# Performance work log

Hardware: AMD Instinct MI355X
Metric: run time of the kernel (lower is better)

The kernel has to match this reference:

```python
import jax, jax.numpy as jnp
import numpy as np

B, M, D, P, T = 512, 16, 128, 16, 4096
GAMMA = 1.0  # similarity_size


def setup_inputs() -> dict:
    key = jax.random.key(0)
    k1, k2, k3, k4, k5 = jax.random.split(key, 5)
    phi = jax.random.normal(k1, (B, P), dtype=jnp.float32)
    state = jax.random.normal(k2, (B, D), dtype=jnp.float32)
    trajectories = jax.random.normal(k3, (T, D), dtype=jnp.float32)
    # Stand-in per-model KAARMA state-transition parameters (linear recurrent + input map, tanh)
    A = jax.random.normal(k4, (M, D, D), dtype=jnp.float32) * (1.0 / np.sqrt(D))
    B_in = jax.random.normal(k5, (M, P, D), dtype=jnp.float32) * (1.0 / np.sqrt(P))
    return {"phi": phi, "state": state, "trajectories": trajectories, "A": A, "B_in": B_in}


def reference(phi, state, trajectories, A, B_in):
    # per-model state update: new_state[b,m,:] = tanh(state @ A_m + phi @ B_m)
    new_state = jnp.tanh(
        jnp.einsum("bd,mdh->bmh", state, A) + jnp.einsum("bp,mph->bmh", phi, B_in)
    )  # [B, M, D]
    # RBF similarity vs trajectory set via ||s||^2 + ||t||^2 - 2 s.t (single batched GEMM)
    s_sq = jnp.sum(new_state * new_state, axis=-1, keepdims=True)      # [B, M, 1]
    t_sq = jnp.sum(trajectories * trajectories, axis=-1)               # [T]
    cross = jnp.einsum("bmd,td->bmt", new_state, trajectories)         # [B, M, T]
    sq_dist = jnp.maximum(s_sq + t_sq[None, None, :] - 2.0 * cross, 0.0)
    sim = jnp.exp(-GAMMA * sq_dist)                                    # [B, M, T]
    output = sim.reshape(phi.shape[0], -1)                             # [B, M*T]
    return output, new_state
```

## Files before the change

kernel.cpp:

```cpp
#include <hip/hip_runtime.h>
#include <hip/hip_bf16.h>
#include <cstdint>
#include <cstddef>

#define NB 512
#define NM 16
#define ND 128
#define NP 16
#define NT 4096

typedef __bf16 bf16x8 __attribute__((ext_vector_type(8)));
typedef float f32x4 __attribute__((ext_vector_type(4)));

static_assert(sizeof(bf16x8) == 16, "bf16x8 must be 16B");

__device__ __forceinline__ void gload_lds16(const void* g, void* l) {
  __builtin_amdgcn_global_load_lds(
      (const __attribute__((address_space(1))) unsigned int*)g,
      (__attribute__((address_space(3))) unsigned int*)l, 16, 0, 0);
}

__global__ __launch_bounds__(256) void prep_kernel(
    const float* __restrict__ phi, const float* __restrict__ state,
    const float* __restrict__ traj, const float* __restrict__ A,
    const float* __restrict__ Bin, float* __restrict__ ns_out,
    __bf16* __restrict__ ns_bf, __bf16* __restrict__ tj_bf,
    float* __restrict__ s_sq, float* __restrict__ t_sq) {
  __shared__ alignas(16) float sSt[16 * 128];
  __shared__ alignas(16) float sPhi[16 * 16];
  __shared__ alignas(16) float sRes[16 * 128];
  const int tid = threadIdx.x;
  const int bx = blockIdx.x;

  if (bx < 512) {
    const int m = bx & 15;
    const int b0 = (bx >> 4) * 16;
    const float4* S4 = (const float4*)(state + (size_t)b0 * 128);
    float4* sSt4 = (float4*)sSt;
    sSt4[tid] = S4[tid];
    sSt4[tid + 256] = S4[tid + 256];
    sPhi[tid] = phi[b0 * 16 + tid];
    __syncthreads();

    const int h2 = tid & 63;
    const int rgrp = tid >> 6;
    const float* Ap = A + (size_t)m * 16384 + h2;
    const float* Bp = Bin + (size_t)m * 2048 + h2;

    float acc[2][4];
#pragma unroll
    for (int hi = 0; hi < 2; ++hi)
#pragma unroll
      for (int j = 0; j < 4; ++j) acc[hi][j] = 0.f;

#pragma unroll 4
    for (int c = 0; c < 32; ++c) {
      float a0[4], a1[4];
#pragma unroll
      for (int u = 0; u < 4; ++u) {
        a0[u] = Ap[(size_t)(c * 4 + u) * 128];
        a1[u] = Ap[(size_t)(c * 4 + u) * 128 + 64];
      }
#pragma unroll
      for (int j = 0; j < 4; ++j) {
        const f32x4 sv = *(const f32x4*)&sSt[(rgrp * 4 + j) * 128 + c * 4];
#pragma unroll
        for (int u = 0; u < 4; ++u) {
          acc[0][j] = fmaf(sv[u], a0[u], acc[0][j]);
          acc[1][j] = fmaf(sv[u], a1[u], acc[1][j]);
        }
      }
    }
#pragma unroll
    for (int pc = 0; pc < 4; ++pc) {
      float b0v[4], b1v[4];
#pragma unroll
      for (int u = 0; u < 4; ++u) {
        b0v[u] = Bp[(size_t)(pc * 4 + u) * 128];
        b1v[u] = Bp[(size_t)(pc * 4 + u) * 128 + 64];
      }
#pragma unroll
      for (int j = 0; j < 4; ++j) {
        const f32x4 pv = *(const f32x4*)&sPhi[(rgrp * 4 + j) * 16 + pc * 4];
#pragma unroll
        for (int u = 0; u < 4; ++u) {
          acc[0][j] = fmaf(pv[u], b0v[u], acc[0][j]);
          acc[1][j] = fmaf(pv[u], b1v[u], acc[1][j]);
        }
      }
    }

#pragma unroll
    for (int j = 0; j < 4; ++j) {
      const int row = rgrp * 4 + j;
      const int R = (b0 + row) * 16 + m;
      const float v0 = tanhf(acc[0][j]);
      const float v1 = tanhf(acc[1][j]);
      ns_out[(size_t)R * 128 + h2] = v0;
      ns_out[(size_t)R * 128 + h2 + 64] = v1;
      sRes[row * 128 + h2] = v0;
      sRes[row * 128 + h2 + 64] = v1;
      float s = v0 * v0 + v1 * v1;
#pragma unroll
      for (int o = 32; o > 0; o >>= 1) s += __shfl_xor(s, o);
      if (h2 == 0) s_sq[R] = s;
    }
    __syncthreads();

    {
      const int row = tid >> 4;
      const int kb = tid & 15;
      const f32x4 r0 = *(const f32x4*)&sRes[row * 128 + kb * 8];
      const f32x4 r1 = *(const f32x4*)&sRes[row * 128 + kb * 8 + 4];
      bf16x8 o;
#pragma unroll
      for (int i = 0; i < 4; ++i) {
        o[i] = (__bf16)r0[i];
        o[i + 4] = (__bf16)r1[i];
      }
      const int R = (b0 + row) * 16 + m;
      *(bf16x8*)(ns_bf + (size_t)R * 128 + ((kb ^ m) * 8)) = o;
    }
  } else {
    const int t0 = (bx - 512) * 128;
    const int t = t0 + (tid >> 1);
    const int half = tid & 1;
    float s = 0.f;
#pragma unroll
    for (int q = 0; q < 8; ++q) {
      const int kb = half * 8 + q;
      const f32x4 v0 = *(const f32x4*)&traj[(size_t)t * 128 + kb * 8];
      const f32x4 v1 = *(const f32x4*)&traj[(size_t)t * 128 + kb * 8 + 4];
      s += v0[0] * v0[0] + v0[1] * v0[1] + v0[2] * v0[2] + v0[3] * v0[3];
      s += v1[0] * v1[0] + v1[1] * v1[1] + v1[2] * v1[2] + v1[3] * v1[3];
      bf16x8 o;
#pragma unroll
      for (int i = 0; i < 4; ++i) {
        o[i] = (__bf16)v0[i];
        o[i + 4] = (__bf16)v1[i];
      }
      *(bf16x8*)(tj_bf + (size_t)t * 128 + ((kb ^ (t & 15)) * 8)) = o;
    }
    s += __shfl_xor(s, 1);
    if (half == 0) t_sq[t] = s;
  }
}

__global__ __launch_bounds__(256) void sim_kernel(
    const __bf16* __restrict__ ns_bf, const __bf16* __restrict__ tj_bf,
    const float* __restrict__ s_sq, const float* __restrict__ t_sq,
    float* __restrict__ out) {
  __shared__ alignas(16) __bf16 sA[128 * 128];
  __shared__ alignas(16) __bf16 sB[128 * 128];
  __shared__ float sSq[128];
  __shared__ float sTq[128];
  const int tid = threadIdx.x;
  const int lane = tid & 63;
  const int w = tid >> 6;
  const int R0 = blockIdx.x * 128;
  const int C0 = blockIdx.y * 128;

  const char* gA = (const char*)(ns_bf + (size_t)R0 * 128);
  const char* gB = (const char*)(tj_bf + (size_t)C0 * 128);
#pragma unroll
  for (int it = 0; it < 8; ++it) {
    const int off = it * 4096 + w * 1024;
    gload_lds16(gA + off + lane * 16, (char*)sA + off);
    gload_lds16(gB + off + lane * 16, (char*)sB + off);
  }
  if (tid < 128)
    sSq[tid] = s_sq[R0 + tid];
  else
    sTq[tid - 128] = t_sq[C0 + tid - 128];
  __syncthreads();

  const int rbase = (w >> 1) * 64;
  const int cbase = (w & 1) * 64;
  const int l15 = lane & 15;
  const int quad = lane >> 4;

  f32x4 acc[4][4];
#pragma unroll
  for (int i = 0; i < 4; ++i)
#pragma unroll
    for (int j = 0; j < 4; ++j) acc[i][j] = (f32x4){0.f, 0.f, 0.f, 0.f};

#pragma unroll
  for (int ks = 0; ks < 4; ++ks) {
    const int kb = quad + ks * 4;
    const int koff = (kb ^ l15) * 8;
    bf16x8 af[4], bfr[4];
#pragma unroll
    for (int i = 0; i < 4; ++i)
      af[i] = *(const bf16x8*)&sA[(rbase + i * 16 + l15) * 128 + koff];
#pragma unroll
    for (int i = 0; i < 4; ++i)
      bfr[i] = *(const bf16x8*)&sB[(cbase + i * 16 + l15) * 128 + koff];
#pragma unroll
    for (int ri = 0; ri < 4; ++ri)
#pragma unroll
      for (int ci = 0; ci < 4; ++ci)
        acc[ri][ci] = __builtin_amdgcn_mfma_f32_16x16x32_bf16(
            bfr[ci], af[ri], acc[ri][ci], 0, 0, 0);
  }

#pragma unroll
  for (int ri = 0; ri < 4; ++ri) {
    const int nsrow = rbase + ri * 16 + l15;
    const float sq = sSq[nsrow];
    float* orow = out + (size_t)(R0 + nsrow) * NT + C0;
#pragma unroll
    for (int ci = 0; ci < 4; ++ci) {
      const int t4 = cbase + ci * 16 + quad * 4;
      const f32x4 tq = *(const f32x4*)&sTq[t4];
      f32x4 r;
#pragma unroll
      for (int k = 0; k < 4; ++k) {
        const float d = fmaxf(sq + tq[k] - 2.f * acc[ri][ci][k], 0.f);
        r[k] = __expf(-d);
      }
      *(f32x4*)&orow[t4] = r;
    }
  }
}

extern "C" void kernel_launch(void* const* d_in, const int* in_sizes, int n_in,
                              void* d_out, int out_size, void* d_ws,
                              size_t ws_size, hipStream_t stream) {
  (void)in_sizes; (void)n_in; (void)out_size; (void)ws_size;
  const float* phi   = (const float*)d_in[0];
  const float* state = (const float*)d_in[1];
  const float* traj  = (const float*)d_in[2];
  const float* A     = (const float*)d_in[3];
  const float* Bin   = (const float*)d_in[4];

  float* out = (float*)d_out;
  float* out_ns = out + (size_t)NB * NM * NT;

  char* ws = (char*)d_ws;
  __bf16* ns_bf = (__bf16*)ws;
  __bf16* tj_bf = (__bf16*)(ws + (2u << 20));
  float* s_sq   = (float*)(ws + (3u << 20));
  float* t_sq   = (float*)(ws + (3u << 20) + (32u << 10));

  prep_kernel<<<544, 256, 0, stream>>>(phi, state, traj, A, Bin, out_ns, ns_bf,
                                       tj_bf, s_sq, t_sq);
  dim3 g2(NB * NM / 128, NT / 128);
  sim_kernel<<<g2, 256, 0, stream>>>(ns_bf, tj_bf, s_sq, t_sq, out);
}
```

Baseline: 168.7 us.

## Stage A in LDS for prep; load MFMA fragments directly from global in sim

The prep kernel now copies each model's A matrix, B_in, and a 32-row state tile into LDS, then computes 4x4 register tiles. It writes bf16 outputs unswizzled, with no second LDS pass. The sim kernel drops its LDS staging and barrier, reads bf16 fragments and norms straight from global/L2, and sets a 3-blocks-per-CU occupancy hint. The aim is to cut repeated global reads of A and LDS/barrier overhead, at the cost of uncoalesced strided global fragment loads and a large LDS footprint in prep.

Result: slower. 180.2 us (+6.8%).

```diff
diff --git a/kernel.cpp b/kernel.cpp
--- a/kernel.cpp
+++ b/kernel.cpp
@@ -10,6 +10,7 @@
 #define NT 4096
 
 typedef __bf16 bf16x8 __attribute__((ext_vector_type(8)));
+typedef __bf16 bf16x4 __attribute__((ext_vector_type(4)));
 typedef float f32x4 __attribute__((ext_vector_type(4)));
 
 static_assert(sizeof(bf16x8) == 16, "bf16x8 must be 16B");
@@ -26,103 +27,104 @@
     const float* __restrict__ Bin, float* __restrict__ ns_out,
     __bf16* __restrict__ ns_bf, __bf16* __restrict__ tj_bf,
     float* __restrict__ s_sq, float* __restrict__ t_sq) {
-  __shared__ alignas(16) float sSt[16 * 128];
-  __shared__ alignas(16) float sPhi[16 * 16];
-  __shared__ alignas(16) float sRes[16 * 128];
+  __shared__ alignas(16) float sA[128 * 128];
+  __shared__ alignas(16) float sB[16 * 128];
+  __shared__ alignas(16) float sSt[32 * 128];
+  __shared__ alignas(16) float sPhi[32 * 16];
   const int tid = threadIdx.x;
   const int bx = blockIdx.x;
-
-  if (bx < 512) {
+  const int lane = tid & 63;
+  const int w = tid >> 6;
+
+  if (bx < 256) {
     const int m = bx & 15;
-    const int b0 = (bx >> 4) * 16;
-    const float4* S4 = (const float4*)(state + (size_t)b0 * 128);
-    float4* sSt4 = (float4*)sSt;
-    sSt4[tid] = S4[tid];
-    sSt4[tid + 256] = S4[tid + 256];
-    sPhi[tid] = phi[b0 * 16 + tid];
+    const int b0 = (bx >> 4) * 32;
+
+    const char* gA = (const char*)(A + (size_t)m * 16384);
+    const char* gB = (const char*)(Bin + (size_t)m * 2048);
+    const char* gS = (const char*)(state + (size_t)b0 * 128);
+#pragma unroll
+    for (int it = 0; it < 16; ++it) {
+      const int off = it * 4096 + w * 1024;
+      gload_lds16(gA + off + lane * 16, (char*)sA + off);
+    }
+#pragma unroll
+    for (int it = 0; it < 2; ++it) {
+      const int off = it * 4096 + w * 1024;
+      gload_lds16(gB + off + lane * 16, (char*)sB + off);
+    }
+#pragma unroll
+    for (int it = 0; it < 4; ++it) {
+      const int off = it * 4096 + w * 1024;
+      gload_lds16(gS + off + lane * 16, (char*)sSt + off);
+    }
+    if (tid < 128)
+      ((float4*)sPhi)[tid] = ((const float4*)(phi + (size_t)b0 * 16))[tid];
     __syncthreads();
 
-    const int h2 = tid & 63;
-    const int rgrp = tid >> 6;
-    const float* Ap = A + (size_t)m * 16384 + h2;
-    const float* Bp = Bin + (size_t)m * 2048 + h2;
-
-    float acc[2][4];
-#pragma unroll
-    for (int hi = 0; hi < 2; ++hi)
-#pragma unroll
-      for (int j = 0; j < 4; ++j) acc[hi][j] = 0.f;
+    const int col4 = (tid & 31) * 4;
+    const int rgrp = tid >> 5;
+    f32x4 acc[4];
+#pragma unroll
+    for (int j = 0; j < 4; ++j) acc[j] = (f32x4){0.f, 0.f, 0.f, 0.f};
 
 #pragma unroll 4
-    for (int c = 0; c < 32; ++c) {
-      float a0[4], a1[4];
-#pragma unroll
-      for (int u = 0; u < 4; ++u) {
-        a0[u] = Ap[(size_t)(c * 4 + u) * 128];
-        a1[u] = Ap[(size_t)(c * 4 + u) * 128 + 64];
-      }
-#pragma unroll
-      for (int j = 0; j < 4; ++j) {
-        const f32x4 sv = *(const f32x4*)&sSt[(rgrp * 4 + j) * 128 + c * 4];
-#pragma unroll
-        for (int u = 0; u < 4; ++u) {
-          acc[0][j] = fmaf(sv[u], a0[u], acc[0][j]);
-          acc[1][j] = fmaf(sv[u], a1[u], acc[1][j]);
-        }
-      }
+    for (int kc = 0; kc < 32; ++kc) {
+      f32x4 av[4], sv[4];
+#pragma unroll
+      for (int u = 0; u < 4; ++u)
+        av[u] = *(const f32x4*)&sA[(kc * 4 + u) * 128 + col4];
+#pragma unroll
+      for (int j = 0; j < 4; ++j)
+        sv[j] = *(const f32x4*)&sSt[(rgrp * 4 + j) * 128 + kc * 4];
+#pragma unroll
+      for (int j = 0; j < 4; ++j)
+#pragma unroll
+        for (int u = 0; u < 4; ++u)
+#pragma unroll
+          for (int c = 0; c < 4; ++c)
+            acc[j][c] = fmaf(sv[j][u], av[u][c], acc[j][c]);
     }
 #pragma unroll
     for (int pc = 0; pc < 4; ++pc) {
-      float b0v[4], b1v[4];
-#pragma unroll
-      for (int u = 0; u < 4; ++u) {
-        b0v[u] = Bp[(size_t)(pc * 4 + u) * 128];
-        b1v[u] = Bp[(size_t)(pc * 4 + u) * 128 + 64];
-      }
-#pragma unroll
-      for (int j = 0; j < 4; ++j) {
-        const f32x4 pv = *(const f32x4*)&sPhi[(rgrp * 4 + j) * 16 + pc * 4];
-#pragma unroll
-        for (int u = 0; u < 4; ++u) {
-          acc[0][j] = fmaf(pv[u], b0v[u], acc[0][j]);
-          acc[1][j] = fmaf(pv[u], b1v[u], acc[1][j]);
-        }
-      }
+      f32x4 bv[4], pv[4];
+#pragma unroll
+      for (int u = 0; u < 4; ++u)
+        bv[u] = *(const f32x4*)&sB[(pc * 4 + u) * 128 + col4];
+#pragma unroll
+      for (int j = 0; j < 4; ++j)
+        pv[j] = *(const f32x4*)&sPhi[(rgrp * 4 + j) * 16 + pc * 4];
+#pragma unroll
+      for (int j = 0; j < 4; ++j)
+#pragma unroll
+        for (int u = 0; u < 4; ++u)
+#pragma unroll
+          for (int c = 0; c < 4; ++c)
+            acc[j][c] = fmaf(pv[j][u], bv[u][c], acc[j][c]);
     }
 
 #pragma unroll
     for (int j = 0; j < 4; ++j) {
       const int row = rgrp * 4 + j;
       const int R = (b0 + row) * 16 + m;
-      const float v0 = tanhf(acc[0][j]);
-      const float v1 = tanhf(acc[1][j]);
-      ns_out[(size_t)R * 128 + h2] = v0;
-      ns_out[(size_t)R * 128 + h2 + 64] = v1;
-      sRes[row * 128 + h2] = v0;
-      sRes[row * 128 + h2 + 64] = v1;
-      float s = v0 * v0 + v1 * v1;
-#pragma unroll
-      for (int o = 32; o > 0; o >>= 1) s += __shfl_xor(s, o);
-      if (h2 == 0) s_sq[R] = s;
-    }
-    __syncthreads();
-
-    {
-      const int row = tid >> 4;
-      const int kb = tid & 15;
-      const f32x4 r0 = *(const f32x4*)&sRes[row * 128 + kb * 8];
-      const f32x4 r1 = *(const f32x4*)&sRes[row * 128 + kb * 8 + 4];
-      bf16x8 o;
-#pragma unroll
-      for (int i = 0; i < 4; ++i) {
-        o[i] = (__bf16)r0[i];
-        o[i + 4] = (__bf16)r1[i];
+      f32x4 v;
+      float ss = 0.f;
+#pragma unroll
+      for (int c = 0; c < 4; ++c) {
+        v[c] = tanhf(acc[j][c]);
+        ss += v[c] * v[c];
       }
-      const int R = (b0 + row) * 16 + m;
-      *(bf16x8*)(ns_bf + (size_t)R * 128 + ((kb ^ m) * 8)) = o;
+      *(f32x4*)&ns_out[(size_t)R * 128 + col4] = v;
+      bf16x4 o;
+#pragma unroll
+      for (int c = 0; c < 4; ++c) o[c] = (__bf16)v[c];
+      *(bf16x4*)(ns_bf + (size_t)R * 128 + col4) = o;
+#pragma unroll
+      for (int o2 = 16; o2 > 0; o2 >>= 1) ss += __shfl_xor(ss, o2);
+      if ((lane & 31) == 0) s_sq[R] = ss;
     }
   } else {
-    const int t0 = (bx - 512) * 128;
+    const int t0 = (bx - 256) * 128;
     const int t = t0 + (tid >> 1);
     const int half = tid & 1;
     float s = 0.f;
@@ -139,46 +141,30 @@
         o[i] = (__bf16)v0[i];
         o[i + 4] = (__bf16)v1[i];
       }
-      *(bf16x8*)(tj_bf + (size_t)t * 128 + ((kb ^ (t & 15)) * 8)) = o;
+      *(bf16x8*)(tj_bf + (size_t)t * 128 + kb * 8) = o;
     }
     s += __shfl_xor(s, 1);
     if (half == 0) t_sq[t] = s;
   }
 }
 
-__global__ __launch_bounds__(256) void sim_kernel(
+__global__ __launch_bounds__(256, 3) void sim_kernel(
     const __bf16* __restrict__ ns_bf, const __bf16* __restrict__ tj_bf,
     const float* __restrict__ s_sq, const float* __restrict__ t_sq,
     float* __restrict__ out) {
-  __shared__ alignas(16) __bf16 sA[128 * 128];
-  __shared__ alignas(16) __bf16 sB[128 * 128];
-  __shared__ float sSq[128];
-  __shared__ float sTq[128];
   const int tid = threadIdx.x;
   const int lane = tid & 63;
   const int w = tid >> 6;
   const int R0 = blockIdx.x * 128;
   const int C0 = blockIdx.y * 128;
-
-  const char* gA = (const char*)(ns_bf + (size_t)R0 * 128);
-  const char* gB = (const char*)(tj_bf + (size_t)C0 * 128);
-#pragma unroll
-  for (int it = 0; it < 8; ++it) {
-    const int off = it * 4096 + w * 1024;
-    gload_lds16(gA + off + lane * 16, (char*)sA + off);
-    gload_lds16(gB + off + lane * 16, (char*)sB + off);
-  }
-  if (tid < 128)
-    sSq[tid] = s_sq[R0 + tid];
-  else
-    sTq[tid - 128] = t_sq[C0 + tid - 128];
-  __syncthreads();
-
   const int rbase = (w >> 1) * 64;
   const int cbase = (w & 1) * 64;
   const int l15 = lane & 15;
   const int quad = lane >> 4;
 
+  const __bf16* Ap = ns_bf + (size_t)(R0 + rbase + l15) * 128 + quad * 8;
+  const __bf16* Bp = tj_bf + (size_t)(C0 + cbase + l15) * 128 + quad * 8;
+
   f32x4 acc[4][4];
 #pragma unroll
   for (int i = 0; i < 4; ++i)
@@ -187,15 +173,13 @@
 
 #pragma unroll
   for (int ks = 0; ks < 4; ++ks) {
-    const int kb = quad + ks * 4;
-    const int koff = (kb ^ l15) * 8;
     bf16x8 af[4], bfr[4];
 #pragma unroll
     for (int i = 0; i < 4; ++i)
-      af[i] = *(const bf16x8*)&sA[(rbase + i * 16 + l15) * 128 + koff];
+      af[i] = *(const bf16x8*)(Ap + i * 2048 + ks * 32);
 #pragma unroll
     for (int i = 0; i < 4; ++i)
-      bfr[i] = *(const bf16x8*)&sB[(cbase + i * 16 + l15) * 128 + koff];
+      bfr[i] = *(const bf16x8*)(Bp + i * 2048 + ks * 32);
 #pragma unroll
     for (int ri = 0; ri < 4; ++ri)
 #pragma unroll
@@ -204,19 +188,22 @@
             bfr[ci], af[ri], acc[ri][ci], 0, 0, 0);
   }
 
+  f32x4 tq[4];
+#pragma unroll
+  for (int ci = 0; ci < 4; ++ci)
+    tq[ci] = *(const f32x4*)&t_sq[C0 + cbase + ci * 16 + quad * 4];
 #pragma unroll
   for (int ri = 0; ri < 4; ++ri) {
     const int nsrow = rbase + ri * 16 + l15;
-    const float sq = sSq[nsrow];
+    const float sq = s_sq[R0 + nsrow];
     float* orow = out + (size_t)(R0 + nsrow) * NT + C0;
 #pragma unroll
     for (int ci = 0; ci < 4; ++ci) {
       const int t4 = cbase + ci * 16 + quad * 4;
-      const f32x4 tq = *(const f32x4*)&sTq[t4];
       f32x4 r;
 #pragma unroll
       for (int k = 0; k < 4; ++k) {
-        const float d = fmaxf(sq + tq[k] - 2.f * acc[ri][ci][k], 0.f);
+        const float d = fmaxf(sq + tq[ci][k] - 2.f * acc[ri][ci][k], 0.f);
         r[k] = __expf(-d);
       }
       *(f32x4*)&orow[t4] = r;
@@ -243,7 +230,7 @@
   float* s_sq   = (float*)(ws + (3u << 20));
   float* t_sq   = (float*)(ws + (3u << 20) + (32u << 10));
 
-  prep_kernel<<<544, 256, 0, stream>>>(phi, state, traj, A, Bin, out_ns, ns_bf,
+  prep_kernel<<<288, 256, 0, stream>>>(phi, state, traj, A, Bin, out_ns, ns_bf,
                                        tj_bf, s_sq, t_sq);
   dim3 g2(NB * NM / 128, NT / 128);
   sim_kernel<<<g2, 256, 0, stream>>>(ns_bf, tj_bf, s_sq, t_sq, out);
```

## Load MFMA operands directly from global memory, dropping LDS staging

Applied to the files above, without the earlier changes.

The sim kernel no longer stages the bf16 state and trajectory tiles into shared memory with global_load_lds and a barrier. Each wave now reads its MFMA fragments straight from global memory (relying on L1/L2 reuse), and the norm vectors come from global memory too. The XOR swizzle in the prep kernel is removed to match, and launch bounds request 3 blocks per SIMD. The aim is to cut the LDS footprint and the barrier so occupancy rises and the output-write-bound kernel overlaps better. The trade-off is that tiles shared between waves are fetched redundantly through the cache.

After: 183.9 us. 1.09x slower.

```diff
diff --git a/kernel.cpp b/kernel.cpp
--- a/kernel.cpp
+++ b/kernel.cpp
@@ -10,15 +10,10 @@
 #define NT 4096
 
 typedef __bf16 bf16x8 __attribute__((ext_vector_type(8)));
+typedef __bf16 bf16x4 __attribute__((ext_vector_type(4)));
 typedef float f32x4 __attribute__((ext_vector_type(4)));
 
 static_assert(sizeof(bf16x8) == 16, "bf16x8 must be 16B");
-
-__device__ __forceinline__ void gload_lds16(const void* g, void* l) {
-  __builtin_amdgcn_global_load_lds(
-      (const __attribute__((address_space(1))) unsigned int*)g,
-      (__attribute__((address_space(3))) unsigned int*)l, 16, 0, 0);
-}
 
 __global__ __launch_bounds__(256) void prep_kernel(
     const float* __restrict__ phi, const float* __restrict__ state,
@@ -119,7 +114,7 @@
         o[i + 4] = (__bf16)r1[i];
       }
       const int R = (b0 + row) * 16 + m;
-      *(bf16x8*)(ns_bf + (size_t)R * 128 + ((kb ^ m) * 8)) = o;
+      *(bf16x8*)(ns_bf + (size_t)R * 128 + kb * 8) = o;
     }
   } else {
     const int t0 = (bx - 512) * 128;
@@ -139,46 +134,30 @@
         o[i] = (__bf16)v0[i];
         o[i + 4] = (__bf16)v1[i];
       }
-      *(bf16x8*)(tj_bf + (size_t)t * 128 + ((kb ^ (t & 15)) * 8)) = o;
+      *(bf16x8*)(tj_bf + (size_t)t * 128 + kb * 8) = o;
     }
     s += __shfl_xor(s, 1);
     if (half == 0) t_sq[t] = s;
   }
 }
 
-__global__ __launch_bounds__(256) void sim_kernel(
+__global__ __launch_bounds__(256, 3) void sim_kernel(
     const __bf16* __restrict__ ns_bf, const __bf16* __restrict__ tj_bf,
     const float* __restrict__ s_sq, const float* __restrict__ t_sq,
     float* __restrict__ out) {
-  __shared__ alignas(16) __bf16 sA[128 * 128];
-  __shared__ alignas(16) __bf16 sB[128 * 128];
-  __shared__ float sSq[128];
-  __shared__ float sTq[128];
   const int tid = threadIdx.x;
   const int lane = tid & 63;
   const int w = tid >> 6;
   const int R0 = blockIdx.x * 128;
   const int C0 = blockIdx.y * 128;
-
-  const char* gA = (const char*)(ns_bf + (size_t)R0 * 128);
-  const char* gB = (const char*)(tj_bf + (size_t)C0 * 128);
-#pragma unroll
-  for (int it = 0; it < 8; ++it) {
-    const int off = it * 4096 + w * 1024;
-    gload_lds16(gA + off + lane * 16, (char*)sA + off);
-    gload_lds16(gB + off + lane * 16, (char*)sB + off);
-  }
-  if (tid < 128)
-    sSq[tid] = s_sq[R0 + tid];
-  else
-    sTq[tid - 128] = t_sq[C0 + tid - 128];
-  __syncthreads();
-
   const int rbase = (w >> 1) * 64;
   const int cbase = (w & 1) * 64;
   const int l15 = lane & 15;
   const int quad = lane >> 4;
 
+  const __bf16* Ap = ns_bf + (size_t)(R0 + rbase + l15) * 128 + quad * 8;
+  const __bf16* Bp = tj_bf + (size_t)(C0 + cbase + l15) * 128 + quad * 8;
+
   f32x4 acc[4][4];
 #pragma unroll
   for (int i = 0; i < 4; ++i)
@@ -187,15 +166,13 @@
 
 #pragma unroll
   for (int ks = 0; ks < 4; ++ks) {
-    const int kb = quad + ks * 4;
-    const int koff = (kb ^ l15) * 8;
     bf16x8 af[4], bfr[4];
 #pragma unroll
     for (int i = 0; i < 4; ++i)
-      af[i] = *(const bf16x8*)&sA[(rbase + i * 16 + l15) * 128 + koff];
+      af[i] = *(const bf16x8*)(Ap + i * 2048 + ks * 32);
 #pragma unroll
     for (int i = 0; i < 4; ++i)
-      bfr[i] = *(const bf16x8*)&sB[(cbase + i * 16 + l15) * 128 + koff];
+      bfr[i] = *(const bf16x8*)(Bp + i * 2048 + ks * 32);
 #pragma unroll
     for (int ri = 0; ri < 4; ++ri)
 #pragma unroll
@@ -204,19 +181,22 @@
             bfr[ci], af[ri], acc[ri][ci], 0, 0, 0);
   }
 
+  f32x4 tq[4];
+#pragma unroll
+  for (int ci = 0; ci < 4; ++ci)
+    tq[ci] = *(const f32x4*)&t_sq[C0 + cbase + ci * 16 + quad * 4];
 #pragma unroll
   for (int ri = 0; ri < 4; ++ri) {
     const int nsrow = rbase + ri * 16 + l15;
-    const float sq = sSq[nsrow];
+    const float sq = s_sq[R0 + nsrow];
     float* orow = out + (size_t)(R0 + nsrow) * NT + C0;
 #pragma unroll
     for (int ci = 0; ci < 4; ++ci) {
       const int t4 = cbase + ci * 16 + quad * 4;
-      const f32x4 tq = *(const f32x4*)&sTq[t4];
       f32x4 r;
 #pragma unroll
       for (int k = 0; k < 4; ++k) {
-        const float d = fmaxf(sq + tq[k] - 2.f * acc[ri][ci][k], 0.f);
+        const float d = fmaxf(sq + tq[ci][k] - 2.f * acc[ri][ci][k], 0.f);
         r[k] = __expf(-d);
       }
       *(f32x4*)&orow[t4] = r;
```
